# Performance work log

Measured on AMD Instinct MI355X. Metric: run time of the kernel, lower is better.

## Reference

```python
import jax, jax.numpy as jnp
import numpy as np

B, C, T = 1024, 64, 275
S = 10            # number of subjects
EMB = 184         # encoder embedding dim
PROJ = 1024       # projector dim
LN_EPS = 1e-5


def setup_inputs() -> dict:
    key = jax.random.key(0)
    ks = jax.random.split(key, 12)
    sc = lambda *shape: 1.0 / np.sqrt(shape[-1] if len(shape) > 1 else 1.0)
    return {
        "eeg": jax.random.normal(ks[0], (B, C, T), dtype=jnp.float32),
        "subject_ids": jax.random.randint(ks[1], (B,), 0, S, dtype=jnp.int64),
        # per-subject Linear(T, T): y = x @ W.T + b
        "subj_W": jax.random.normal(ks[2], (S, T, T), dtype=jnp.float32) / np.sqrt(T),
        "subj_b": jax.random.normal(ks[3], (S, T), dtype=jnp.float32) * 0.02,
        # encoder stub: flatten (C*T) -> Linear -> EMB
        "enc_W": jax.random.normal(ks[4], (C * T, EMB), dtype=jnp.float32) / np.sqrt(C * T),
        "enc_b": jnp.zeros((EMB,), dtype=jnp.float32),
        # projector: Linear(EMB, PROJ) -> ResidualAdd(GELU -> Linear(PROJ, PROJ)) -> LayerNorm
        "W1": jax.random.normal(ks[5], (EMB, PROJ), dtype=jnp.float32) / np.sqrt(EMB),
        "b1": jnp.zeros((PROJ,), dtype=jnp.float32),
        "W2": jax.random.normal(ks[6], (PROJ, PROJ), dtype=jnp.float32) / np.sqrt(PROJ),
        "b2": jnp.zeros((PROJ,), dtype=jnp.float32),
        "gamma": jnp.ones((PROJ,), dtype=jnp.float32),
        "beta": jnp.zeros((PROJ,), dtype=jnp.float32),
    }


def reference(eeg, subject_ids, subj_W, subj_b, enc_W, enc_b, W1, b1, W2, b2, gamma, beta):
    # --- subject-wise alignment: grouped gather -> linear -> scatter ---
    # Vectorized form of the per-subject loop: each row b uses weight subj_W[sid[b]].
    Wg = subj_W[subject_ids]              # [B, T, T]
    bg = subj_b[subject_ids]              # [B, T]
    # torch Linear: y = x @ W.T + b  ->  y[b,c,u] = sum_t eeg[b,c,t] * Wg[b,u,t]
    x = jnp.einsum("bct,but->bcu", eeg, Wg) + bg[:, None, :]   # [B, C, T]

    # --- encoder stub (SpatioTemporalCNN placeholder): flatten + linear ---
    h = x.reshape(x.shape[0], -1) @ enc_W + enc_b              # [B, EMB]

    # --- MLPProjector ---
    h = h @ W1 + b1                                            # [B, PROJ]
    r = jax.nn.gelu(h, approximate=False) @ W2 + b2            # dropout is identity at eval
    h = h + r
    # LayerNorm over last dim
    mu = jnp.mean(h, axis=-1, keepdims=True)
    var = jnp.mean(jnp.square(h - mu), axis=-1, keepdims=True)
    out = (h - mu) * jax.lax.rsqrt(var + LN_EPS) * gamma + beta
    return out
```

## Files before the change

### kernel.cpp

```cpp
#include <hip/hip_runtime.h>
#include <math.h>

#define B_N    1024
#define C_N    64
#define T_N    275
#define S_N    10
#define EMB_N  184
#define PROJ_N 1024
#define CT_N   (C_N * T_N)
#define TP     288
#define KP2    (C_N * TP)
#define EMBP   192
#define KZ2    16
#define KC2    (KP2 / KZ2)
#define KZ5    2
#define GMAX   264

#define SEC_W   0
#define SEC_E   810
#define SEC_1   1002
#define SEC_2   1050
#define SEC_G   1306
#define SEC_N   1307

typedef unsigned short u16;
typedef __attribute__((ext_vector_type(8))) short short8;
typedef __attribute__((ext_vector_type(4))) short short4v;
typedef __attribute__((ext_vector_type(4))) float f32x4;

#define MFMA16(a,b,c) __builtin_amdgcn_mfma_f32_16x16x32_bf16(a, b, c, 0, 0, 0)

__device__ __forceinline__ u16 f2bf(float f) {
    union { float f; unsigned u; } v; v.f = f;
    unsigned r = v.u + 0x7FFFu + ((v.u >> 16) & 1u);
    return (u16)(r >> 16);
}
__device__ __forceinline__ float gelu_exact(float v) {
    return 0.5f * v * (1.0f + erff(v * 0.70710678118654752f));
}
__device__ __forceinline__ void gload16(const void* g, void* lds) {
    __builtin_amdgcn_global_load_lds(
        (const __attribute__((address_space(1))) void*)g,
        (__attribute__((address_space(3))) void*)lds, 16, 0, 0);
}

__global__ __launch_bounds__(256) void p_all(
    const int* __restrict__ sid, const float* __restrict__ W,
    const float* __restrict__ encW, const float* __restrict__ W1,
    const float* __restrict__ W2, const float* __restrict__ subj_b,
    u16* __restrict__ Wb, u16* __restrict__ eT, u16* __restrict__ w1t,
    u16* __restrict__ w2t, int* __restrict__ bsq, float* __restrict__ sbp)
{
    __shared__ char smem[16640];
    const int blk = blockIdx.x;
    const int tid = threadIdx.x;

    if (blk < SEC_E) {
        int idx4 = blk * 256 + tid;
        if (idx4 >= S_N * TP * TP / 4) return;
        int o = idx4 * 4;
        int row = o / TP, t = o - row * TP;
        int s = row / TP, u = row - s * TP;
        short4v pk;
        #pragma unroll
        for (int e = 0; e < 4; ++e) {
            float v = (u < T_N && t + e < T_N)
                ? W[((size_t)s * T_N + u) * T_N + t + e] : 0.f;
            pk[e] = (short)f2bf(v);
        }
        *reinterpret_cast<short4v*>(Wb + o) = pk;
        return;
    }
    if (blk < SEC_1) {
        float (*tile)[65] = (float(*)[65])smem;
        int local = blk - SEC_E;
        const int c = local / 3;
        const int n0 = (local % 3) * 64;
        for (int u0 = 0; u0 < TP; u0 += 64) {
            int wlen = (TP - u0 < 64) ? (TP - u0) : 64;
            __syncthreads();
            for (int l = tid; l < 4096; l += 256) {
                int i = l >> 6, j = l & 63;
                int u = u0 + i, n = n0 + j;
                float v = 0.f;
                if (u < T_N && n < EMB_N)
                    v = encW[((size_t)c * T_N + u) * EMB_N + n];
                tile[i][j] = v;
            }
            __syncthreads();
            for (int l = tid; l < 4096; l += 256) {
                int j = l >> 6, i = l & 63;
                if (i < wlen)
                    eT[(size_t)(n0 + j) * KP2 + (size_t)c * TP + u0 + i] =
                        f2bf(tile[i][j]);
            }
        }
        return;
    }
    if (blk < SEC_2) {
        float (*tile)[65] = (float(*)[65])smem;
        int local = blk - SEC_1;
        const int k0 = (local % 3) * 64, n0 = (local / 3) * 64;
        for (int l = tid; l < 4096; l += 256) {
            int i = l >> 6, j = l & 63;
            float v = (k0 + i < EMB_N) ? W1[(size_t)(k0 + i) * PROJ_N + n0 + j] : 0.f;
            tile[i][j] = v;
        }
        __syncthreads();
        for (int l = tid; l < 4096; l += 256) {
            int j = l >> 6, i = l & 63;
            w1t[(size_t)(n0 + j) * EMBP + k0 + i] = f2bf(tile[i][j]);
        }
        return;
    }
    if (blk < SEC_G) {
        float (*tile)[65] = (float(*)[65])smem;
        int local = blk - SEC_2;
        const int k0 = (local % 16) * 64, n0 = (local / 16) * 64;
        for (int l = tid; l < 4096; l += 256) {
            int i = l >> 6, j = l & 63;
            tile[i][j] = W2[(size_t)(k0 + i) * PROJ_N + n0 + j];
        }
        __syncthreads();
        for (int l = tid; l < 4096; l += 256) {
            int j = l >> 6, i = l & 63;
            w2t[(size_t)(n0 + j) * PROJ_N + k0 + i] = f2bf(tile[i][j]);
        }
        return;
    }
    {
        for (int i = tid; i < S_N * TP; i += 256) {
            int s = i / TP, u = i - s * TP;
            sbp[i] = (u < T_N) ? subj_b[s * T_N + u] : 0.f;
        }
        int* sgrp = (int*)smem;
        int* C    = (int*)(smem + 4096);
        int* tot  = (int*)(smem + 4096 + 640);
        for (int i = tid; i < 1024; i += 256) sgrp[i] = sid[i];
        for (int i = tid; i < 4 * GMAX; i += 256) bsq[i] = -1;
        __syncthreads();
        const int w4 = tid >> 6, lane = tid & 63;
        #pragma unroll
        for (int j = 0; j < 4; ++j) {
            int chunk = w4 * 4 + j;
            int sb = sgrp[chunk * 64 + lane];
            int myc = 0;
            for (int s = 0; s < S_N; ++s) {
                unsigned long long m = __ballot(sb == s);
                if (lane == s) myc = (int)__popcll(m);
            }
            if (lane < S_N) C[chunk * S_N + lane] = myc;
        }
        __syncthreads();
        if (tid < S_N) {
            int a = 0;
            for (int w2 = 0; w2 < 16; ++w2) a += C[w2 * S_N + tid];
            tot[tid] = a;
        }
        __syncthreads();
        #pragma unroll
        for (int rep = 0; rep < 4; ++rep) {
            int b = tid + rep * 256;
            int s = sgrp[b];
            int off = 0;
            for (int s2 = 0; s2 < S_N; ++s2)
                if (s2 < s) off += (tot[s2] + 3) & ~3;
            int chunk = b >> 6;
            int rank = 0;
            for (int w2 = 0; w2 < 16; ++w2)
                if (w2 < chunk) rank += C[w2 * S_N + s];
            for (int i = chunk * 64; i < b; ++i) rank += (sgrp[i] == s) ? 1 : 0;
            bsq[off + rank] = b;
        }
    }
}

__global__ __launch_bounds__(256, 3) void k1g(
    const float* __restrict__ eeg, const int* __restrict__ sid,
    const u16* __restrict__ Wb, const float* __restrict__ sbp,
    const int* __restrict__ bsq, u16* __restrict__ xb)
{
    __shared__ __align__(16) u16 Ws[2][TP * 32];
    __shared__ __align__(16) u16 Es[2][64 * 40];
    const int g = blockIdx.x;
    const int b0 = bsq[g * 4];
    if (b0 < 0) return;
    const int p = blockIdx.y >> 1, ch = blockIdx.y & 1;
    const int s = sid[b0];
    const int tid = threadIdx.x;
    const int w = tid >> 6, lane = tid & 63;
    const int bi = w >> 1, uh = w & 1;
    const int lrow = lane & 15, lk = lane >> 4;
    const int b = bsq[g * 4 + p * 2 + bi];
    const u16* Wr = Wb + (size_t)s * TP * TP;

    const int srow = tid >> 2;
    const int quarter = tid & 3;
    const int bt = srow >> 5, cl = srow & 31;
    int bstage = bsq[g * 4 + p * 2 + bt]; if (bstage < 0) bstage = b0;
    const float* esrc = eeg + (size_t)bstage * CT_N + (ch * 32 + cl) * T_N;

    #define K1_WSTAGE(st, ks)                                                  \
        for (int l = tid; l < TP * 4; l += 256) {                              \
            int u_ = l >> 2, q_ = l & 3;                                       \
            gload16(Wr + (size_t)u_ * TP + (ks) * 32 + ((q_ ^ ((u_ >> 1) & 3)) << 3), \
                    &Ws[st][l * 8]);                                           \
        }
    #define K1_ELOAD(ks, v)                                                    \
        {   int t0_ = (ks) * 32 + quarter * 8;                                 \
            if (t0_ + 8 <= T_N) {                                              \
                __builtin_memcpy(&v[0], esrc + t0_, 32);                       \
            } else {                                                           \
                _Pragma("unroll")                                              \
                for (int e = 0; e < 8; ++e)                                    \
                    v[e] = (t0_ + e < T_N) ? esrc[t0_ + e] : 0.f;              \
            }                                                                  \
        }
    #define K1_EWRITE(st, v)                                                   \
        {   short8 pk_;                                                        \
            _Pragma("unroll")                                                  \
            for (int e = 0; e < 8; ++e) pk_[e] = (short)f2bf(v[e]);            \
            *reinterpret_cast<short8*>(&Es[st][srow * 40 + quarter * 8]) = pk_;\
        }

    f32x4 acc[9][2] = {};
    float ev[8], evn[8];

    K1_WSTAGE(0, 0);
    K1_ELOAD(0, ev);
    K1_EWRITE(0, ev);
    __syncthreads();

    for (int ks = 0; ks < 9; ++ks) {
        const int st = ks & 1;
        if (ks < 8) {
            K1_WSTAGE(st ^ 1, ks + 1);
            K1_ELOAD(ks + 1, evn);
        }
        short8 ef[2];
        #pragma unroll
        for (int rt = 0; rt < 2; ++rt)
            ef[rt] = *reinterpret_cast<const short8*>(
                &Es[st][(bi * 32 + rt * 16 + lrow) * 40 + lk * 8]);
        #pragma unroll
        for (int uf = 0; uf < 9; ++uf) {
            int u = uh * 144 + uf * 16 + lrow;
            int chunk = u * 4 + (lk ^ ((u >> 1) & 3));
            short8 av = *reinterpret_cast<const short8*>(&Ws[st][chunk * 8]);
            #pragma unroll
            for (int rt = 0; rt < 2; ++rt)
                acc[uf][rt] = MFMA16(av, ef[rt], acc[uf][rt]);
        }
        if (ks < 8) K1_EWRITE(st ^ 1, evn);
        __syncthreads();
    }

    if (b < 0) return;
    u16* xrow = xb + (size_t)b * KP2 + (size_t)(ch * 32) * TP;
    #pragma unroll
    for (int uf = 0; uf < 9; ++uf) {
        int ub = uh * 144 + uf * 16 + 4 * lk;
        float4 b4 = *reinterpret_cast<const float4*>(sbp + s * TP + ub);
        float bias[4] = { b4.x, b4.y, b4.z, b4.w };
        #pragma unroll
        for (int rt = 0; rt < 2; ++rt) {
            int c = rt * 16 + lrow;
            short4v pk;
            #pragma unroll
            for (int r = 0; r < 4; ++r)
                pk[r] = (ub + r < T_N) ? (short)f2bf(acc[uf][rt][r] + bias[r])
                                       : (short)0;
            *reinterpret_cast<short4v*>(xrow + (size_t)c * TP + ub) = pk;
        }
    }
    #undef K1_WSTAGE
    #undef K1_ELOAD
    #undef K1_EWRITE
}

__global__ __launch_bounds__(256) void k2_mfma(
    const u16* __restrict__ xb, const u16* __restrict__ eT,
    float* __restrict__ part)
{
    __shared__ __align__(16) u16 Ab[2][64 * 64];
    const int m0 = blockIdx.x * 64;
    const int kz = blockIdx.y;
    const int kbase = kz * KC2;
    const int tid = threadIdx.x;
    const int w = tid >> 6, lane = tid & 63;
    const int lrow = lane & 15, lk = lane >> 4;

    #define K2_STAGE(st, step)                                                 \
        _Pragma("unroll")                                                      \
        for (int p = 0; p < 2; ++p) {                                          \
            int l = tid + p * 256;                                             \
            int r_ = l >> 3, q_ = l & 7;                                       \
            gload16(xb + (size_t)(m0 + r_) * KP2 + kbase + (step) * 64 +       \
                        ((q_ ^ (r_ & 7)) << 3),                                \
                    &Ab[st][l * 8]);                                           \
        }
    #define K2_BLOAD(step, dst)                                                \
        _Pragma("unroll")                                                      \
        for (int ct = 0; ct < 3; ++ct)                                         \
            _Pragma("unroll")                                                  \
            for (int ki = 0; ki < 2; ++ki)                                     \
                dst[ct][ki] = *reinterpret_cast<const short8*>(                \
                    eT + (size_t)(48 * w + 16 * ct + lrow) * KP2 + kbase +     \
                    (step) * 64 + ki * 32 + 8 * lk);

    f32x4 acc[4][3] = {};
    short8 bf[3][2], bn[3][2];

    K2_STAGE(0, 0);
    K2_BLOAD(0, bf);
    __syncthreads();

    for (int step = 0; step < 18; ++step) {
        const int st = step & 1;
        if (step < 17) {
            K2_STAGE(st ^ 1, step + 1);
            K2_BLOAD(step + 1, bn);
        }
        #pragma unroll
        for (int ki = 0; ki < 2; ++ki)
            #pragma unroll
            for (int rt = 0; rt < 4; ++rt) {
                int m = 16 * rt + lrow;
                int chunk = m * 8 + ((4 * ki + lk) ^ (m & 7));
                short8 af = *reinterpret_cast<const short8*>(&Ab[st][chunk * 8]);
                #pragma unroll
                for (int ct = 0; ct < 3; ++ct)
                    acc[rt][ct] = MFMA16(af, bf[ct][ki], acc[rt][ct]);
            }
        __syncthreads();
        #pragma unroll
        for (int ct = 0; ct < 3; ++ct)
            #pragma unroll
            for (int ki = 0; ki < 2; ++ki) bf[ct][ki] = bn[ct][ki];
    }

    #pragma unroll
    for (int rt = 0; rt < 4; ++rt)
        #pragma unroll
        for (int ct = 0; ct < 3; ++ct) {
            int n = 48 * w + 16 * ct + lrow;
            #pragma unroll
            for (int r = 0; r < 4; ++r) {
                int m = m0 + 16 * rt + 4 * lk + r;
                part[((size_t)kz * B_N + m) * EMBP + n] = acc[rt][ct][r];
            }
        }
    #undef K2_STAGE
    #undef K2_BLOAD
}

__global__ __launch_bounds__(256) void k3_reduce(
    const float* __restrict__ part, const float* __restrict__ enc_b,
    u16* __restrict__ hb)
{
    int idx = blockIdx.x * 256 + threadIdx.x;
    if (idx >= B_N * EMBP) return;
    int n = idx % EMBP;
    float s = 0.f;
    if (n < EMB_N) {
        s = enc_b[n];
        #pragma unroll
        for (int z = 0; z < KZ2; ++z)
            s += part[(size_t)z * B_N * EMBP + idx];
    }
    hb[idx] = f2bf(s);
}

__global__ __launch_bounds__(256) void k4_mfma(
    const u16* __restrict__ hb, const u16* __restrict__ w1t,
    const float* __restrict__ b1, float* __restrict__ h1, u16* __restrict__ g)
{
    __shared__ __align__(16) u16 Ab[64 * EMBP];
    __shared__ __align__(16) u16 Bb[64 * EMBP];
    const int m0 = blockIdx.x * 64, n0 = blockIdx.y * 64;
    const int tid = threadIdx.x;
    const int w = tid >> 6, lane = tid & 63;
    const int wr = w >> 1, wc = w & 1;
    const int lrow = lane & 15, lk = lane >> 4;

    #pragma unroll
    for (int i = 0; i < 6; ++i) {
        int L = tid + i * 256;
        int row = L / 24, qp = L % 24;
        int ql = qp ^ (row & 7);
        gload16(hb  + (size_t)(m0 + row) * EMBP + ql * 8, &Ab[(size_t)L * 8]);
        gload16(w1t + (size_t)(n0 + row) * EMBP + ql * 8, &Bb[(size_t)L * 8]);
    }
    __syncthreads();

    f32x4 acc[2][2] = {};
    #pragma unroll
    for (int ks = 0; ks < 6; ++ks) {
        #pragma unroll
        for (int rt = 0; rt < 2; ++rt) {
            int c = 32 * wr + 16 * rt + lrow;
            short8 af = *reinterpret_cast<const short8*>(
                &Ab[c * EMBP + (((4 * ks + lk) ^ (c & 7)) * 8)]);
            #pragma unroll
            for (int ct = 0; ct < 2; ++ct) {
                int nl = 32 * wc + 16 * ct + lrow;
                short8 bfv = *reinterpret_cast<const short8*>(
                    &Bb[nl * EMBP + (((4 * ks + lk) ^ (nl & 7)) * 8)]);
                acc[rt][ct] = MFMA16(af, bfv, acc[rt][ct]);
            }
        }
    }
    #pragma unroll
    for (int rt = 0; rt < 2; ++rt)
        #pragma unroll
        for (int ct = 0; ct < 2; ++ct) {
            int n = n0 + 32 * wc + 16 * ct + lrow;
            #pragma unroll
            for (int r = 0; r < 4; ++r) {
                int m = m0 + 32 * wr + 16 * rt + 4 * lk + r;
                float v = acc[rt][ct][r] + b1[n];
                size_t o = (size_t)m * PROJ_N + n;
                h1[o] = v;
                g[o] = f2bf(gelu_exact(v));
            }
        }
}

__global__ __launch_bounds__(256) void k5_mfma(
    const u16* __restrict__ g, const u16* __restrict__ w2t,
    float* __restrict__ part2)
{
    __shared__ __align__(16) u16 Ab[2][64 * 64];
    __shared__ __align__(16) u16 Bb[2][64 * 64];
    const int m0 = blockIdx.x * 64, n0 = blockIdx.y * 64;
    const int kz = blockIdx.z;
    const int kbase = kz * (PROJ_N / KZ5);
    const int tid = threadIdx.x;
    const int w = tid >> 6, lane = tid & 63;
    const int wr = w >> 1, wc = w & 1;
    const int lrow = lane & 15, lk = lane >> 4;

    const int r0 = tid >> 3, q0 = tid & 7;
    const int r1 = (tid + 256) >> 3;
    const u16* a0 = g + (size_t)(m0 + r0) * PROJ_N + (q0 ^ (r0 & 7)) * 8;
    const u16* a1 = g + (size_t)(m0 + r1) * PROJ_N + (q0 ^ (r1 & 7)) * 8;
    const u16* b0 = w2t + (size_t)(n0 + r0) * PROJ_N + (q0 ^ (r0 & 7)) * 8;
    const u16* b1p = w2t + (size_t)(n0 + r1) * PROJ_N + (q0 ^ (r1 & 7)) * 8;

    f32x4 acc[2][2] = {};
    int buf = 0;
    gload16(a0 + kbase, &Ab[0][(size_t)(w * 64) * 8]);
    gload16(a1 + kbase, &Ab[0][(size_t)(w * 64 + 256) * 8]);
    gload16(b0 + kbase, &Bb[0][(size_t)(w * 64) * 8]);
    gload16(b1p + kbase, &Bb[0][(size_t)(w * 64 + 256) * 8]);
    __syncthreads();

    for (int step = 0; step < 8; ++step) {
        if (step < 7) {
            int k0 = kbase + (step + 1) * 64;
            gload16(a0 + k0, &Ab[buf ^ 1][(size_t)(w * 64) * 8]);
            gload16(a1 + k0, &Ab[buf ^ 1][(size_t)(w * 64 + 256) * 8]);
            gload16(b0 + k0, &Bb[buf ^ 1][(size_t)(w * 64) * 8]);
            gload16(b1p + k0, &Bb[buf ^ 1][(size_t)(w * 64 + 256) * 8]);
        }
        #pragma unroll
        for (int ki = 0; ki < 2; ++ki) {
            #pragma unroll
            for (int rt = 0; rt < 2; ++rt) {
                int c = 32 * wr + 16 * rt + lrow;
                short8 af = *reinterpret_cast<const short8*>(
                    &Ab[buf][c * 64 + (((lk + 4 * ki) ^ (c & 7)) * 8)]);
                #pragma unroll
                for (int ct = 0; ct < 2; ++ct) {
                    int nl = 32 * wc + 16 * ct + lrow;
                    short8 bfv = *reinterpret_cast<const short8*>(
                        &Bb[buf][nl * 64 + (((lk + 4 * ki) ^ (nl & 7)) * 8)]);
                    acc[rt][ct] = MFMA16(af, bfv, acc[rt][ct]);
                }
            }
        }
        __syncthreads();
        buf ^= 1;
    }
    #pragma unroll
    for (int rt = 0; rt < 2; ++rt)
        #pragma unroll
        for (int ct = 0; ct < 2; ++ct) {
            int n = n0 + 32 * wc + 16 * ct + lrow;
            #pragma unroll
            for (int r = 0; r < 4; ++r) {
                int m = m0 + 32 * wr + 16 * rt + 4 * lk + r;
                part2[(size_t)kz * B_N * PROJ_N + (size_t)m * PROJ_N + n] = acc[rt][ct][r];
            }
        }
}

__global__ __launch_bounds__(256) void k5r_ln(
    const float* __restrict__ part2, const float* __restrict__ h1,
    const float* __restrict__ b2, const float* __restrict__ gamma,
    const float* __restrict__ beta, float* __restrict__ out)
{
    const int m = blockIdx.x;
    const int tid = threadIdx.x;
    const float4* h4 = reinterpret_cast<const float4*>(h1 + (size_t)m * PROJ_N);
    const float4* p0 = reinterpret_cast<const float4*>(part2 + (size_t)m * PROJ_N);
    const float4* p1 = reinterpret_cast<const float4*>(part2 + (size_t)(B_N + m) * PROJ_N);
    const float4* b4 = reinterpret_cast<const float4*>(b2);
    float4 va = h4[tid], vb = p0[tid], vc = p1[tid], vd = b4[tid];
    float v[4] = { va.x + vb.x + vc.x + vd.x, va.y + vb.y + vc.y + vd.y,
                   va.z + vb.z + vc.z + vd.z, va.w + vb.w + vc.w + vd.w };
    float s = 0.f, sq = 0.f;
    #pragma unroll
    for (int i = 0; i < 4; ++i) { s += v[i]; sq += v[i] * v[i]; }
    #pragma unroll
    for (int off = 32; off > 0; off >>= 1) {
        s  += __shfl_down(s, off);
        sq += __shfl_down(sq, off);
    }
    __shared__ float ss[4], ssq[4];
    int wid = tid >> 6, lane = tid & 63;
    if (lane == 0) { ss[wid] = s; ssq[wid] = sq; }
    __syncthreads();
    if (tid == 0) {
        float a = 0.f, bsum = 0.f;
        #pragma unroll
        for (int q = 0; q < 4; ++q) { a += ss[q]; bsum += ssq[q]; }
        ss[0] = a; ssq[0] = bsum;
    }
    __syncthreads();
    float mu  = ss[0] * (1.0f / PROJ_N);
    float var = ssq[0] * (1.0f / PROJ_N) - mu * mu;
    float rs  = rsqrtf(var + 1e-5f);
    const float4 g4 = reinterpret_cast<const float4*>(gamma)[tid];
    const float4 be4 = reinterpret_cast<const float4*>(beta)[tid];
    float gg[4] = { g4.x, g4.y, g4.z, g4.w };
    float bb[4] = { be4.x, be4.y, be4.z, be4.w };
    float4 o4;
    float* op = reinterpret_cast<float*>(&o4);
    #pragma unroll
    for (int i = 0; i < 4; ++i) op[i] = (v[i] - mu) * rs * gg[i] + bb[i];
    reinterpret_cast<float4*>(out + (size_t)m * PROJ_N)[tid] = o4;
}

extern "C" void kernel_launch(void* const* d_in, const int* in_sizes, int n_in,
                              void* d_out, int out_size, void* d_ws, size_t ws_size,
                              hipStream_t stream)
{
    const float* eeg    = (const float*)d_in[0];
    const int*   sid    = (const int*)  d_in[1];
    const float* subj_W = (const float*)d_in[2];
    const float* subj_b = (const float*)d_in[3];
    const float* enc_W  = (const float*)d_in[4];
    const float* enc_b  = (const float*)d_in[5];
    const float* W1     = (const float*)d_in[6];
    const float* b1     = (const float*)d_in[7];
    const float* W2     = (const float*)d_in[8];
    const float* b2     = (const float*)d_in[9];
    const float* gamma  = (const float*)d_in[10];
    const float* beta   = (const float*)d_in[11];
    float* out = (float*)d_out;

    char* w = (char*)d_ws;
    u16*   xb    = (u16*)(w);
    u16*   Wb    = (u16*)(w + 37748736);
    u16*   eT    = (u16*)(w + 39407616);
    u16*   w1t   = (u16*)(w + 46485504);
    u16*   w2t   = (u16*)(w + 46878720);
    u16*   hb    = (u16*)(w + 48975872);
    float* h1    = (float*)(w + 49369088);
    u16*   g     = (u16*)(w + 53563392);
    float* sbp   = (float*)(w + 55660544);
    int*   bsq   = (int*)(w + 55672064);
    float* part  = (float*)(w + 55676288);
    float* part2 = (float*)(w + 68259200);

    p_all<<<dim3(SEC_N), 256, 0, stream>>>(sid, subj_W, enc_W, W1, W2, subj_b,
                                           Wb, eT, w1t, w2t, bsq, sbp);
    k1g  <<<dim3(GMAX, 4), 256, 0, stream>>>(eeg, sid, Wb, sbp, bsq, xb);
    k2_mfma<<<dim3(16, KZ2), 256, 0, stream>>>(xb, eT, part);
    k3_reduce<<<dim3((B_N * EMBP + 255) / 256), 256, 0, stream>>>(part, enc_b, hb);
    k4_mfma<<<dim3(16, 16), 256, 0, stream>>>(hb, w1t, b1, h1, g);
    k5_mfma<<<dim3(16, 16, KZ5), 256, 0, stream>>>(g, w2t, part2);
    k5r_ln <<<dim3(B_N), 256, 0, stream>>>(part2, h1, b2, gamma, beta, out);
}
```

Before: 120.0 us.

## Load subject-linear operands straight to registers, dropping LDS staging and barriers

The subject-alignment kernel no longer stages the weight and EEG tiles through double-buffered shared memory. Each lane now loads its MFMA fragments directly from global memory into registers, with a one-step register prefetch, and all __syncthreads are gone. This trades LDS traffic and barrier stalls for redundant global/L2 reads, since waves sharing weights or EEG rows now each fetch them, and it raises register pressure under the occupancy-3 launch bound. EEG loads become scalar per-element reads rather than vectorized.

```diff
diff --git a/kernel.cpp b/kernel.cpp
--- a/kernel.cpp
+++ b/kernel.cpp
@@ -42,6 +42,12 @@
     __builtin_amdgcn_global_load_lds(
         (const __attribute__((address_space(1))) void*)g,
         (__attribute__((address_space(3))) void*)lds, 16, 0, 0);
+}
+__device__ __forceinline__ short8 cv8(const float* v) {
+    short8 r;
+    #pragma unroll
+    for (int e = 0; e < 8; ++e) r[e] = (short)f2bf(v[e]);
+    return r;
 }
 
 __global__ __launch_bounds__(256) void p_all(
@@ -175,13 +181,11 @@
     }
 }
 
-__global__ __launch_bounds__(256, 3) void k1g(
+__global__ __launch_bounds__(256, 3) void k1d(
     const float* __restrict__ eeg, const int* __restrict__ sid,
     const u16* __restrict__ Wb, const float* __restrict__ sbp,
     const int* __restrict__ bsq, u16* __restrict__ xb)
 {
-    __shared__ __align__(16) u16 Ws[2][TP * 32];
-    __shared__ __align__(16) u16 Es[2][64 * 40];
     const int g = blockIdx.x;
     const int b0 = bsq[g * 4];
     if (b0 < 0) return;
@@ -192,67 +196,52 @@
     const int bi = w >> 1, uh = w & 1;
     const int lrow = lane & 15, lk = lane >> 4;
     const int b = bsq[g * 4 + p * 2 + bi];
-    const u16* Wr = Wb + (size_t)s * TP * TP;
-
-    const int srow = tid >> 2;
-    const int quarter = tid & 3;
-    const int bt = srow >> 5, cl = srow & 31;
-    int bstage = bsq[g * 4 + p * 2 + bt]; if (bstage < 0) bstage = b0;
-    const float* esrc = eeg + (size_t)bstage * CT_N + (ch * 32 + cl) * T_N;
-
-    #define K1_WSTAGE(st, ks)                                                  \
-        for (int l = tid; l < TP * 4; l += 256) {                              \
-            int u_ = l >> 2, q_ = l & 3;                                       \
-            gload16(Wr + (size_t)u_ * TP + (ks) * 32 + ((q_ ^ ((u_ >> 1) & 3)) << 3), \
-                    &Ws[st][l * 8]);                                           \
-        }
-    #define K1_ELOAD(ks, v)                                                    \
-        {   int t0_ = (ks) * 32 + quarter * 8;                                 \
-            if (t0_ + 8 <= T_N) {                                              \
-                __builtin_memcpy(&v[0], esrc + t0_, 32);                       \
+    const int bs = (b >= 0) ? b : b0;
+
+    const float* e0 = eeg + (size_t)bs * CT_N + (ch * 32 + lrow) * T_N;
+    const float* e1 = e0 + 16 * T_N;
+    const u16* Wr = Wb + (size_t)s * TP * TP + (size_t)(uh * 144 + lrow) * TP;
+
+    #define K1_ELOAD(ks)                                                       \
+        {   const int tbase = (ks) * 32 + lk * 8;                              \
+            if ((ks) < 8) {                                                    \
+                _Pragma("unroll")                                              \
+                for (int e = 0; e < 8; ++e) {                                  \
+                    ea[e] = e0[tbase + e];                                     \
+                    eb[e] = e1[tbase + e];                                     \
+                }                                                              \
             } else {                                                           \
                 _Pragma("unroll")                                              \
-                for (int e = 0; e < 8; ++e)                                    \
-                    v[e] = (t0_ + e < T_N) ? esrc[t0_ + e] : 0.f;              \
+                for (int e = 0; e < 8; ++e) {                                  \
+                    int t_ = tbase + e;                                        \
+                    ea[e] = (t_ < T_N) ? e0[t_] : 0.f;                         \
+                    eb[e] = (t_ < T_N) ? e1[t_] : 0.f;                         \
+                }                                                              \
             }                                                                  \
         }
-    #define K1_EWRITE(st, v)                                                   \
-        {   short8 pk_;                                                        \
-            _Pragma("unroll")                                                  \
-            for (int e = 0; e < 8; ++e) pk_[e] = (short)f2bf(v[e]);            \
-            *reinterpret_cast<short8*>(&Es[st][srow * 40 + quarter * 8]) = pk_;\
-        }
+    #define K1_WLOAD(ks)                                                       \
+        _Pragma("unroll")                                                      \
+        for (int uf = 0; uf < 9; ++uf)                                         \
+            wv[uf] = *reinterpret_cast<const short8*>(                         \
+                Wr + (size_t)uf * 16 * TP + (ks) * 32 + lk * 8);
 
     f32x4 acc[9][2] = {};
-    float ev[8], evn[8];
-
-    K1_WSTAGE(0, 0);
-    K1_ELOAD(0, ev);
-    K1_EWRITE(0, ev);
-    __syncthreads();
-
+    float ea[8], eb[8];
+    short8 wv[9];
+
+    K1_ELOAD(0);
+    K1_WLOAD(0);
+
+    #pragma unroll
     for (int ks = 0; ks < 9; ++ks) {
-        const int st = ks & 1;
-        if (ks < 8) {
-            K1_WSTAGE(st ^ 1, ks + 1);
-            K1_ELOAD(ks + 1, evn);
-        }
-        short8 ef[2];
-        #pragma unroll
-        for (int rt = 0; rt < 2; ++rt)
-            ef[rt] = *reinterpret_cast<const short8*>(
-                &Es[st][(bi * 32 + rt * 16 + lrow) * 40 + lk * 8]);
+        short8 ef0 = cv8(ea), ef1 = cv8(eb);
+        if (ks < 8) K1_ELOAD(ks + 1);
         #pragma unroll
         for (int uf = 0; uf < 9; ++uf) {
-            int u = uh * 144 + uf * 16 + lrow;
-            int chunk = u * 4 + (lk ^ ((u >> 1) & 3));
-            short8 av = *reinterpret_cast<const short8*>(&Ws[st][chunk * 8]);
-            #pragma unroll
-            for (int rt = 0; rt < 2; ++rt)
-                acc[uf][rt] = MFMA16(av, ef[rt], acc[uf][rt]);
-        }
-        if (ks < 8) K1_EWRITE(st ^ 1, evn);
-        __syncthreads();
+            acc[uf][0] = MFMA16(wv[uf], ef0, acc[uf][0]);
+            acc[uf][1] = MFMA16(wv[uf], ef1, acc[uf][1]);
+        }
+        if (ks < 8) K1_WLOAD(ks + 1);
     }
 
     if (b < 0) return;
@@ -263,19 +252,18 @@
         float4 b4 = *reinterpret_cast<const float4*>(sbp + s * TP + ub);
         float bias[4] = { b4.x, b4.y, b4.z, b4.w };
         #pragma unroll
-        for (int rt = 0; rt < 2; ++rt) {
-            int c = rt * 16 + lrow;
+        for (int cf = 0; cf < 2; ++cf) {
+            int c = cf * 16 + lrow;
             short4v pk;
             #pragma unroll
             for (int r = 0; r < 4; ++r)
-                pk[r] = (ub + r < T_N) ? (short)f2bf(acc[uf][rt][r] + bias[r])
+                pk[r] = (ub + r < T_N) ? (short)f2bf(acc[uf][cf][r] + bias[r])
                                        : (short)0;
             *reinterpret_cast<short4v*>(xrow + (size_t)c * TP + ub) = pk;
         }
     }
-    #undef K1_WSTAGE
     #undef K1_ELOAD
-    #undef K1_EWRITE
+    #undef K1_WLOAD
 }
 
 __global__ __launch_bounds__(256) void k2_mfma(
@@ -576,7 +564,7 @@
 
     p_all<<<dim3(SEC_N), 256, 0, stream>>>(sid, subj_W, enc_W, W1, W2, subj_b,
                                            Wb, eT, w1t, w2t, bsq, sbp);
-    k1g  <<<dim3(GMAX, 4), 256, 0, stream>>>(eeg, sid, Wb, sbp, bsq, xb);
+    k1d  <<<dim3(GMAX, 4), 256, 0, stream>>>(eeg, sid, Wb, sbp, bsq, xb);
     k2_mfma<<<dim3(16, KZ2), 256, 0, stream>>>(xb, eT, part);
     k3_reduce<<<dim3((B_N * EMBP + 255) / 256), 256, 0, stream>>>(part, enc_b, hb);
     k4_mfma<<<dim3(16, 16), 256, 0, stream>>>(hb, w1t, b1, h1, g);
```

After: 135.7 us. +13.1%, slower.
